# Performance work log

Measured on AMD Instinct MI355X. Metric: run time of the kernel, lower is better.

## Reference

```python
import jax, jax.numpy as jnp
import numpy as np

EPS = 1e-8  # torch CosineSimilarity eps


def setup_inputs() -> dict:
    key = jax.random.key(0)
    ks = jax.random.split(key, 7)
    N, D, H = 8192, 3, 256
    return {
        "pattern1": jax.random.normal(ks[0], (D,), jnp.float32),
        "pattern2": jax.random.normal(ks[1], (D,), jnp.float32),
        "working_memory": jax.random.normal(ks[2], (N, D), jnp.float32),
        "Wp": jax.random.normal(ks[3], (H, D), jnp.float32) * 0.1,
        "bp": jax.random.normal(ks[4], (H,), jnp.float32) * 0.1,
        "Wq": jax.random.normal(ks[5], (H, D), jnp.float32) * 0.1,
        "bq": jax.random.normal(ks[6], (H,), jnp.float32) * 0.1,
    }


def reference(pattern1, pattern2, working_memory, Wp, bp, Wq, bq):
    # Embed patterns and all propositions (torch Linear: x @ W.T + b)
    p1 = pattern1 @ Wp.T + bp                       # (H,)
    p2 = pattern2 @ Wp.T + bp                       # (H,)
    props = working_memory @ Wq.T + bq              # (N, H)
    prop_norm = jnp.linalg.norm(props, axis=-1)     # (N,)

    def match(pemb):
        # sigmoid(cosine_sim(pemb, props))  -> (N,)
        num = props @ pemb
        den = jnp.maximum(prop_norm * jnp.linalg.norm(pemb), EPS)
        return jax.nn.sigmoid(num / den)

    m1 = match(p1)                                  # (N,)
    m2 = match(p2)                                  # (N,)

    # Entity-link: cosine sim of scalar wm[i,2] with wm[j,0]
    obj = working_memory[:, 2]                      # (N,)
    subj = working_memory[:, 0]                     # (N,)
    num = obj[:, None] * subj[None, :]              # (N, N)
    den = jnp.maximum(jnp.abs(obj)[:, None] * jnp.abs(subj)[None, :], EPS)
    link = jax.nn.sigmoid(num / den)                # (N, N)

    out = m1[:, None] * m2[None, :] * link          # (N, N)
    N = out.shape[0]
    # zero the diagonal (i != j in the original loop)
    return out * (1.0 - jnp.eye(N, dtype=out.dtype))
```

## Files before the change

kernel.cpp:

```cpp
#include <hip/hip_runtime.h>
#include <math.h>

#define EPS 1e-8f
constexpr int N = 8192;
constexpr int ROWS_PER_BLOCK = 8;
constexpr int COLS_PER_BLOCK = 1024;
constexpr float LPOS = 0.7310585786300049f;
constexpr float LNEG = 0.2689414213699951f;

__global__ __launch_bounds__(256) void match_kernel(
    const float* __restrict__ pat1, const float* __restrict__ pat2,
    const float* __restrict__ Wp, const float* __restrict__ bp,
    const float* __restrict__ wm, const float* __restrict__ Wq,
    const float* __restrict__ bq,
    float4* __restrict__ rowpack, float* __restrict__ m2,
    float* __restrict__ subj) {
  const int row = (blockIdx.x * blockDim.x + threadIdx.x) >> 6;
  const int lane = threadIdx.x & 63;
  const float a0 = pat1[0], a1 = pat1[1], a2 = pat1[2];
  const float b0 = pat2[0], b1 = pat2[1], b2 = pat2[2];
  const float x0 = wm[row * 3 + 0];
  const float x1 = wm[row * 3 + 1];
  const float x2 = wm[row * 3 + 2];
  float s0 = 0.f, s1 = 0.f, s2 = 0.f, n1 = 0.f, n2 = 0.f;
#pragma unroll
  for (int k = 0; k < 4; ++k) {
    const int h = lane + k * 64;
    const float wp0 = Wp[h * 3 + 0], wp1 = Wp[h * 3 + 1], wp2 = Wp[h * 3 + 2];
    const float bph = bp[h];
    const float v1 = fmaf(wp0, a0, fmaf(wp1, a1, fmaf(wp2, a2, bph)));
    const float v2 = fmaf(wp0, b0, fmaf(wp1, b1, fmaf(wp2, b2, bph)));
    const float v  = fmaf(Wq[h * 3 + 0], x0,
                     fmaf(Wq[h * 3 + 1], x1,
                     fmaf(Wq[h * 3 + 2], x2, bq[h])));
    s0 = fmaf(v, v, s0);
    s1 = fmaf(v, v1, s1);
    s2 = fmaf(v, v2, s2);
    n1 = fmaf(v1, v1, n1);
    n2 = fmaf(v2, v2, n2);
  }
#pragma unroll
  for (int off = 32; off > 0; off >>= 1) {
    s0 += __shfl_xor(s0, off, 64);
    s1 += __shfl_xor(s1, off, 64);
    s2 += __shfl_xor(s2, off, 64);
    n1 += __shfl_xor(n1, off, 64);
    n2 += __shfl_xor(n2, off, 64);
  }
  if (lane == 0) {
    const float pn = sqrtf(s0);
    const float d1 = fmaxf(pn * sqrtf(n1), EPS);
    const float d2 = fmaxf(pn * sqrtf(n2), EPS);
    const float mm1 = 1.f / (1.f + __expf(-(s1 / d1)));
    const float mm2 = 1.f / (1.f + __expf(-(s2 / d2)));
    m2[row]   = mm2;
    subj[row] = x0;
    float4 rp;
    rp.x = mm1;
    rp.y = x2;
    rp.z = EPS / fabsf(x2);
    rp.w = 0.f;
    rowpack[row] = rp;
  }
}

__device__ __forceinline__ float exact_elem(float a, float oi, float m2c,
                                            float sjc) {
  const float t = oi * sjc;
  const float z = t / fmaxf(fabsf(t), EPS);
  return a * m2c * (1.f / (1.f + __expf(-z)));
}

__global__ __launch_bounds__(256) void outer_kernel(
    const float4* __restrict__ rowpack, const float* __restrict__ m2,
    const float* __restrict__ subj, float* __restrict__ out) {
  const int jBase = blockIdx.x * COLS_PER_BLOCK + threadIdx.x * 4;
  const int iBase = blockIdx.y * ROWS_PER_BLOCK;
  const float4 m2v = *reinterpret_cast<const float4*>(m2 + jBase);
  const float4 sjv = *reinterpret_cast<const float4*>(subj + jBase);
  float4 qp, qm, asj;
  qp.x = m2v.x * (sjv.x > 0.f ? LPOS : LNEG);
  qp.y = m2v.y * (sjv.y > 0.f ? LPOS : LNEG);
  qp.z = m2v.z * (sjv.z > 0.f ? LPOS : LNEG);
  qp.w = m2v.w * (sjv.w > 0.f ? LPOS : LNEG);
  qm.x = m2v.x * (sjv.x > 0.f ? LNEG : LPOS);
  qm.y = m2v.y * (sjv.y > 0.f ? LNEG : LPOS);
  qm.z = m2v.z * (sjv.z > 0.f ? LNEG : LPOS);
  qm.w = m2v.w * (sjv.w > 0.f ? LNEG : LPOS);
  asj.x = fabsf(sjv.x);
  asj.y = fabsf(sjv.y);
  asj.z = fabsf(sjv.z);
  asj.w = fabsf(sjv.w);
  const float minasj = fminf(fminf(asj.x, asj.y), fminf(asj.z, asj.w));
  const bool diagTile = (iBase >> 10) == (int)blockIdx.x;
#pragma unroll
  for (int r = 0; r < ROWS_PER_BLOCK; ++r) {
    const int i = iBase + r;
    const float4 rp = rowpack[i];
    const float a = rp.x, oi = rp.y, thr = rp.z;
    const bool neg = oi < 0.f;
    float4 o;
    o.x = a * (neg ? qm.x : qp.x);
    o.y = a * (neg ? qm.y : qp.y);
    o.z = a * (neg ? qm.z : qp.z);
    o.w = a * (neg ? qm.w : qp.w);
    if (__builtin_expect(__any(minasj < thr), 0)) {
      if (asj.x < thr) o.x = exact_elem(a, oi, m2v.x, sjv.x);
      if (asj.y < thr) o.y = exact_elem(a, oi, m2v.y, sjv.y);
      if (asj.z < thr) o.z = exact_elem(a, oi, m2v.z, sjv.z);
      if (asj.w < thr) o.w = exact_elem(a, oi, m2v.w, sjv.w);
    }
    if (diagTile) {
      if (jBase + 0 == i) o.x = 0.f;
      if (jBase + 1 == i) o.y = 0.f;
      if (jBase + 2 == i) o.z = 0.f;
      if (jBase + 3 == i) o.w = 0.f;
    }
    *reinterpret_cast<float4*>(out + (size_t)i * N + jBase) = o;
  }
}

extern "C" void kernel_launch(void* const* d_in, const int* in_sizes, int n_in,
                              void* d_out, int out_size, void* d_ws,
                              size_t ws_size, hipStream_t stream) {
  const float* pat1 = (const float*)d_in[0];
  const float* pat2 = (const float*)d_in[1];
  const float* wm   = (const float*)d_in[2];
  const float* Wp   = (const float*)d_in[3];
  const float* bp   = (const float*)d_in[4];
  const float* Wq   = (const float*)d_in[5];
  const float* bq   = (const float*)d_in[6];
  float* out = (float*)d_out;

  float4* rowpack = (float4*)d_ws;
  float* m2   = (float*)(rowpack + N);
  float* subj = m2 + N;

  match_kernel<<<N / 4, 256, 0, stream>>>(pat1, pat2, Wp, bp, wm, Wq, bq,
                                          rowpack, m2, subj);
  dim3 grid(N / COLS_PER_BLOCK, N / ROWS_PER_BLOCK);
  outer_kernel<<<grid, 256, 0, stream>>>(rowpack, m2, subj, out);
}
```

Before: 50.22 us.

## Restructure outer kernel to one block per output row

The outer-product kernel now gives each block a whole output row, looping over 8 column chunks of 1024. Previously each block handled 8 rows by 1024 columns and reused column data held in registers. Now each block reads the row scalars once and reloads the column vectors (m2, subj) from cache in every chunk. This trades column-data reuse in registers for a simpler per-row schedule and contiguous row writes. Output is 256MB and store-bound either way.

```diff
diff --git a/kernel.cpp b/kernel.cpp
--- a/kernel.cpp
+++ b/kernel.cpp
@@ -3,8 +3,6 @@
 
 #define EPS 1e-8f
 constexpr int N = 8192;
-constexpr int ROWS_PER_BLOCK = 8;
-constexpr int COLS_PER_BLOCK = 1024;
 constexpr float LPOS = 0.7310585786300049f;
 constexpr float LNEG = 0.2689414213699951f;
 
@@ -74,49 +72,39 @@
 __global__ __launch_bounds__(256) void outer_kernel(
     const float4* __restrict__ rowpack, const float* __restrict__ m2,
     const float* __restrict__ subj, float* __restrict__ out) {
-  const int jBase = blockIdx.x * COLS_PER_BLOCK + threadIdx.x * 4;
-  const int iBase = blockIdx.y * ROWS_PER_BLOCK;
-  const float4 m2v = *reinterpret_cast<const float4*>(m2 + jBase);
-  const float4 sjv = *reinterpret_cast<const float4*>(subj + jBase);
-  float4 qp, qm, asj;
-  qp.x = m2v.x * (sjv.x > 0.f ? LPOS : LNEG);
-  qp.y = m2v.y * (sjv.y > 0.f ? LPOS : LNEG);
-  qp.z = m2v.z * (sjv.z > 0.f ? LPOS : LNEG);
-  qp.w = m2v.w * (sjv.w > 0.f ? LPOS : LNEG);
-  qm.x = m2v.x * (sjv.x > 0.f ? LNEG : LPOS);
-  qm.y = m2v.y * (sjv.y > 0.f ? LNEG : LPOS);
-  qm.z = m2v.z * (sjv.z > 0.f ? LNEG : LPOS);
-  qm.w = m2v.w * (sjv.w > 0.f ? LNEG : LPOS);
-  asj.x = fabsf(sjv.x);
-  asj.y = fabsf(sjv.y);
-  asj.z = fabsf(sjv.z);
-  asj.w = fabsf(sjv.w);
-  const float minasj = fminf(fminf(asj.x, asj.y), fminf(asj.z, asj.w));
-  const bool diagTile = (iBase >> 10) == (int)blockIdx.x;
+  const int i = blockIdx.x;
+  const float4 rp = rowpack[i];
+  const float a = rp.x, oi = rp.y, thr = rp.z;
+  const float aLP = a * LPOS;
+  const float aLN = a * LNEG;
+  const bool neg = oi < 0.f;
+  float* __restrict__ outrow = out + (size_t)i * N;
+  const int t4 = threadIdx.x * 4;
 #pragma unroll
-  for (int r = 0; r < ROWS_PER_BLOCK; ++r) {
-    const int i = iBase + r;
-    const float4 rp = rowpack[i];
-    const float a = rp.x, oi = rp.y, thr = rp.z;
-    const bool neg = oi < 0.f;
+  for (int c = 0; c < N / 1024; ++c) {
+    const int j = c * 1024 + t4;
+    const float4 m2v = *reinterpret_cast<const float4*>(m2 + j);
+    const float4 sjv = *reinterpret_cast<const float4*>(subj + j);
     float4 o;
-    o.x = a * (neg ? qm.x : qp.x);
-    o.y = a * (neg ? qm.y : qp.y);
-    o.z = a * (neg ? qm.z : qp.z);
-    o.w = a * (neg ? qm.w : qp.w);
-    if (__builtin_expect(__any(minasj < thr), 0)) {
-      if (asj.x < thr) o.x = exact_elem(a, oi, m2v.x, sjv.x);
-      if (asj.y < thr) o.y = exact_elem(a, oi, m2v.y, sjv.y);
-      if (asj.z < thr) o.z = exact_elem(a, oi, m2v.z, sjv.z);
-      if (asj.w < thr) o.w = exact_elem(a, oi, m2v.w, sjv.w);
+    o.x = m2v.x * (((sjv.x > 0.f) != neg) ? aLP : aLN);
+    o.y = m2v.y * (((sjv.y > 0.f) != neg) ? aLP : aLN);
+    o.z = m2v.z * (((sjv.z > 0.f) != neg) ? aLP : aLN);
+    o.w = m2v.w * (((sjv.w > 0.f) != neg) ? aLP : aLN);
+    const float mn = fminf(fminf(fabsf(sjv.x), fabsf(sjv.y)),
+                           fminf(fabsf(sjv.z), fabsf(sjv.w)));
+    if (__builtin_expect(__any(mn < thr), 0)) {
+      if (fabsf(sjv.x) < thr) o.x = exact_elem(a, oi, m2v.x, sjv.x);
+      if (fabsf(sjv.y) < thr) o.y = exact_elem(a, oi, m2v.y, sjv.y);
+      if (fabsf(sjv.z) < thr) o.z = exact_elem(a, oi, m2v.z, sjv.z);
+      if (fabsf(sjv.w) < thr) o.w = exact_elem(a, oi, m2v.w, sjv.w);
     }
-    if (diagTile) {
-      if (jBase + 0 == i) o.x = 0.f;
-      if (jBase + 1 == i) o.y = 0.f;
-      if (jBase + 2 == i) o.z = 0.f;
-      if (jBase + 3 == i) o.w = 0.f;
+    if (__builtin_expect((unsigned)(i - j) < 4u, 0)) {
+      if (j + 0 == i) o.x = 0.f;
+      if (j + 1 == i) o.y = 0.f;
+      if (j + 2 == i) o.z = 0.f;
+      if (j + 3 == i) o.w = 0.f;
     }
-    *reinterpret_cast<float4*>(out + (size_t)i * N + jBase) = o;
+    *reinterpret_cast<float4*>(outrow + j) = o;
   }
 }
 
@@ -138,6 +126,5 @@
 
   match_kernel<<<N / 4, 256, 0, stream>>>(pat1, pat2, Wp, bp, wm, Wq, bq,
                                           rowpack, m2, subj);
-  dim3 grid(N / COLS_PER_BLOCK, N / ROWS_PER_BLOCK);
-  outer_kernel<<<grid, 256, 0, stream>>>(rowpack, m2, subj, out);
+  outer_kernel<<<N, 256, 0, stream>>>(rowpack, m2, subj, out);
 }
```

Result: no change. 51.10 us (+1.8%).

## Fuse match and outer kernels into one cooperative persistent kernel with grid sync

Applied to the files above, without the earlier changes.

Merges the match and outer-product kernels into a single cooperative launch of 1024 persistent blocks. Each block first computes row embeddings and match scores, then a grid-wide sync runs before it loops over output tiles in a grid-stride pattern. This removes the second kernel launch and the inter-kernel gap. In exchange it adds a grid barrier, the overhead of a cooperative launch, and less parallelism in the match phase, since each block now handles 8 rows.

```diff
diff --git a/kernel.cpp b/kernel.cpp
--- a/kernel.cpp
+++ b/kernel.cpp
@@ -1,68 +1,19 @@
 #include <hip/hip_runtime.h>
+#include <hip/hip_cooperative_groups.h>
 #include <math.h>
+
+namespace cg = cooperative_groups;
 
 #define EPS 1e-8f
 constexpr int N = 8192;
-constexpr int ROWS_PER_BLOCK = 8;
-constexpr int COLS_PER_BLOCK = 1024;
+constexpr int NBLOCKS = 1024;
+constexpr int ROWS_PER_TILE = 8;
+constexpr int COLS_PER_TILE = 1024;
+constexpr int NSTRIPES = N / COLS_PER_TILE;
+constexpr int NTILES = (N / ROWS_PER_TILE) * NSTRIPES;
+constexpr int TILES_PER_BLOCK = NTILES / NBLOCKS;
 constexpr float LPOS = 0.7310585786300049f;
 constexpr float LNEG = 0.2689414213699951f;
-
-__global__ __launch_bounds__(256) void match_kernel(
-    const float* __restrict__ pat1, const float* __restrict__ pat2,
-    const float* __restrict__ Wp, const float* __restrict__ bp,
-    const float* __restrict__ wm, const float* __restrict__ Wq,
-    const float* __restrict__ bq,
-    float4* __restrict__ rowpack, float* __restrict__ m2,
-    float* __restrict__ subj) {
-  const int row = (blockIdx.x * blockDim.x + threadIdx.x) >> 6;
-  const int lane = threadIdx.x & 63;
-  const float a0 = pat1[0], a1 = pat1[1], a2 = pat1[2];
-  const float b0 = pat2[0], b1 = pat2[1], b2 = pat2[2];
-  const float x0 = wm[row * 3 + 0];
-  const float x1 = wm[row * 3 + 1];
-  const float x2 = wm[row * 3 + 2];
-  float s0 = 0.f, s1 = 0.f, s2 = 0.f, n1 = 0.f, n2 = 0.f;
-#pragma unroll
-  for (int k = 0; k < 4; ++k) {
-    const int h = lane + k * 64;
-    const float wp0 = Wp[h * 3 + 0], wp1 = Wp[h * 3 + 1], wp2 = Wp[h * 3 + 2];
-    const float bph = bp[h];
-    const float v1 = fmaf(wp0, a0, fmaf(wp1, a1, fmaf(wp2, a2, bph)));
-    const float v2 = fmaf(wp0, b0, fmaf(wp1, b1, fmaf(wp2, b2, bph)));
-    const float v  = fmaf(Wq[h * 3 + 0], x0,
-                     fmaf(Wq[h * 3 + 1], x1,
-                     fmaf(Wq[h * 3 + 2], x2, bq[h])));
-    s0 = fmaf(v, v, s0);
-    s1 = fmaf(v, v1, s1);
-    s2 = fmaf(v, v2, s2);
-    n1 = fmaf(v1, v1, n1);
-    n2 = fmaf(v2, v2, n2);
-  }
-#pragma unroll
-  for (int off = 32; off > 0; off >>= 1) {
-    s0 += __shfl_xor(s0, off, 64);
-    s1 += __shfl_xor(s1, off, 64);
-    s2 += __shfl_xor(s2, off, 64);
-    n1 += __shfl_xor(n1, off, 64);
-    n2 += __shfl_xor(n2, off, 64);
-  }
-  if (lane == 0) {
-    const float pn = sqrtf(s0);
-    const float d1 = fmaxf(pn * sqrtf(n1), EPS);
-    const float d2 = fmaxf(pn * sqrtf(n2), EPS);
-    const float mm1 = 1.f / (1.f + __expf(-(s1 / d1)));
-    const float mm2 = 1.f / (1.f + __expf(-(s2 / d2)));
-    m2[row]   = mm2;
-    subj[row] = x0;
-    float4 rp;
-    rp.x = mm1;
-    rp.y = x2;
-    rp.z = EPS / fabsf(x2);
-    rp.w = 0.f;
-    rowpack[row] = rp;
-  }
-}
 
 __device__ __forceinline__ float exact_elem(float a, float oi, float m2c,
                                             float sjc) {
@@ -71,52 +22,121 @@
   return a * m2c * (1.f / (1.f + __expf(-z)));
 }
 
-__global__ __launch_bounds__(256) void outer_kernel(
-    const float4* __restrict__ rowpack, const float* __restrict__ m2,
-    const float* __restrict__ subj, float* __restrict__ out) {
-  const int jBase = blockIdx.x * COLS_PER_BLOCK + threadIdx.x * 4;
-  const int iBase = blockIdx.y * ROWS_PER_BLOCK;
-  const float4 m2v = *reinterpret_cast<const float4*>(m2 + jBase);
-  const float4 sjv = *reinterpret_cast<const float4*>(subj + jBase);
-  float4 qp, qm, asj;
-  qp.x = m2v.x * (sjv.x > 0.f ? LPOS : LNEG);
-  qp.y = m2v.y * (sjv.y > 0.f ? LPOS : LNEG);
-  qp.z = m2v.z * (sjv.z > 0.f ? LPOS : LNEG);
-  qp.w = m2v.w * (sjv.w > 0.f ? LPOS : LNEG);
-  qm.x = m2v.x * (sjv.x > 0.f ? LNEG : LPOS);
-  qm.y = m2v.y * (sjv.y > 0.f ? LNEG : LPOS);
-  qm.z = m2v.z * (sjv.z > 0.f ? LNEG : LPOS);
-  qm.w = m2v.w * (sjv.w > 0.f ? LNEG : LPOS);
-  asj.x = fabsf(sjv.x);
-  asj.y = fabsf(sjv.y);
-  asj.z = fabsf(sjv.z);
-  asj.w = fabsf(sjv.w);
-  const float minasj = fminf(fminf(asj.x, asj.y), fminf(asj.z, asj.w));
-  const bool diagTile = (iBase >> 10) == (int)blockIdx.x;
+__global__ __launch_bounds__(256, 4) void fused_kernel(
+    const float* __restrict__ pat1, const float* __restrict__ pat2,
+    const float* __restrict__ Wp, const float* __restrict__ bp,
+    const float* __restrict__ wm, const float* __restrict__ Wq,
+    const float* __restrict__ bq,
+    float4* __restrict__ rowpack, float* __restrict__ m2arr,
+    float* __restrict__ subjarr, float* __restrict__ out) {
+  const int wid = threadIdx.x >> 6;
+  const int lane = threadIdx.x & 63;
+
+  {
+    const float a0 = pat1[0], a1 = pat1[1], a2 = pat1[2];
+    const float b0 = pat2[0], b1 = pat2[1], b2 = pat2[2];
 #pragma unroll
-  for (int r = 0; r < ROWS_PER_BLOCK; ++r) {
-    const int i = iBase + r;
-    const float4 rp = rowpack[i];
-    const float a = rp.x, oi = rp.y, thr = rp.z;
-    const bool neg = oi < 0.f;
-    float4 o;
-    o.x = a * (neg ? qm.x : qp.x);
-    o.y = a * (neg ? qm.y : qp.y);
-    o.z = a * (neg ? qm.z : qp.z);
-    o.w = a * (neg ? qm.w : qp.w);
-    if (__builtin_expect(__any(minasj < thr), 0)) {
-      if (asj.x < thr) o.x = exact_elem(a, oi, m2v.x, sjv.x);
-      if (asj.y < thr) o.y = exact_elem(a, oi, m2v.y, sjv.y);
-      if (asj.z < thr) o.z = exact_elem(a, oi, m2v.z, sjv.z);
-      if (asj.w < thr) o.w = exact_elem(a, oi, m2v.w, sjv.w);
+    for (int rr = 0; rr < 2; ++rr) {
+      const int row = blockIdx.x * 8 + rr * 4 + wid;
+      const float x0 = wm[row * 3 + 0];
+      const float x1 = wm[row * 3 + 1];
+      const float x2 = wm[row * 3 + 2];
+      float s0 = 0.f, s1 = 0.f, s2 = 0.f, n1 = 0.f, n2 = 0.f;
+#pragma unroll
+      for (int k = 0; k < 4; ++k) {
+        const int h = lane + k * 64;
+        const float wp0 = Wp[h * 3 + 0], wp1 = Wp[h * 3 + 1],
+                    wp2 = Wp[h * 3 + 2];
+        const float bph = bp[h];
+        const float v1 = fmaf(wp0, a0, fmaf(wp1, a1, fmaf(wp2, a2, bph)));
+        const float v2 = fmaf(wp0, b0, fmaf(wp1, b1, fmaf(wp2, b2, bph)));
+        const float v  = fmaf(Wq[h * 3 + 0], x0,
+                         fmaf(Wq[h * 3 + 1], x1,
+                         fmaf(Wq[h * 3 + 2], x2, bq[h])));
+        s0 = fmaf(v, v, s0);
+        s1 = fmaf(v, v1, s1);
+        s2 = fmaf(v, v2, s2);
+        n1 = fmaf(v1, v1, n1);
+        n2 = fmaf(v2, v2, n2);
+      }
+#pragma unroll
+      for (int off = 32; off > 0; off >>= 1) {
+        s0 += __shfl_xor(s0, off, 64);
+        s1 += __shfl_xor(s1, off, 64);
+        s2 += __shfl_xor(s2, off, 64);
+        n1 += __shfl_xor(n1, off, 64);
+        n2 += __shfl_xor(n2, off, 64);
+      }
+      if (lane == 0) {
+        const float pn = sqrtf(s0);
+        const float d1 = fmaxf(pn * sqrtf(n1), EPS);
+        const float d2 = fmaxf(pn * sqrtf(n2), EPS);
+        const float mm1 = 1.f / (1.f + __expf(-(s1 / d1)));
+        const float mm2 = 1.f / (1.f + __expf(-(s2 / d2)));
+        m2arr[row]   = mm2;
+        subjarr[row] = x0;
+        float4 rp;
+        rp.x = mm1;
+        rp.y = x2;
+        rp.z = EPS / fabsf(x2);
+        rp.w = 0.f;
+        rowpack[row] = rp;
+      }
     }
-    if (diagTile) {
-      if (jBase + 0 == i) o.x = 0.f;
-      if (jBase + 1 == i) o.y = 0.f;
-      if (jBase + 2 == i) o.z = 0.f;
-      if (jBase + 3 == i) o.w = 0.f;
+  }
+
+  __threadfence();
+  cg::this_grid().sync();
+
+#pragma unroll 1
+  for (int k = 0; k < TILES_PER_BLOCK; ++k) {
+    const int t = blockIdx.x + k * NBLOCKS;
+    const int bx = t & (NSTRIPES - 1);
+    const int by = t >> 3;
+    const int jBase = bx * COLS_PER_TILE + (int)threadIdx.x * 4;
+    const int iBase = by * ROWS_PER_TILE;
+    const float4 m2v = *reinterpret_cast<const float4*>(m2arr + jBase);
+    const float4 sjv = *reinterpret_cast<const float4*>(subjarr + jBase);
+    float4 qp, qm, asj;
+    qp.x = m2v.x * (sjv.x > 0.f ? LPOS : LNEG);
+    qp.y = m2v.y * (sjv.y > 0.f ? LPOS : LNEG);
+    qp.z = m2v.z * (sjv.z > 0.f ? LPOS : LNEG);
+    qp.w = m2v.w * (sjv.w > 0.f ? LPOS : LNEG);
+    qm.x = m2v.x * (sjv.x > 0.f ? LNEG : LPOS);
+    qm.y = m2v.y * (sjv.y > 0.f ? LNEG : LPOS);
+    qm.z = m2v.z * (sjv.z > 0.f ? LNEG : LPOS);
+    qm.w = m2v.w * (sjv.w > 0.f ? LNEG : LPOS);
+    asj.x = fabsf(sjv.x);
+    asj.y = fabsf(sjv.y);
+    asj.z = fabsf(sjv.z);
+    asj.w = fabsf(sjv.w);
+    const float minasj = fminf(fminf(asj.x, asj.y), fminf(asj.z, asj.w));
+    const bool diagTile = (iBase >> 10) == bx;
+#pragma unroll
+    for (int r = 0; r < ROWS_PER_TILE; ++r) {
+      const int i = iBase + r;
+      const float4 rp = rowpack[i];
+      const float a = rp.x, oi = rp.y, thr = rp.z;
+      const bool neg = oi < 0.f;
+      float4 o;
+      o.x = a * (neg ? qm.x : qp.x);
+      o.y = a * (neg ? qm.y : qp.y);
+      o.z = a * (neg ? qm.z : qp.z);
+      o.w = a * (neg ? qm.w : qp.w);
+      if (__builtin_expect(__any(minasj < thr), 0)) {
+        if (asj.x < thr) o.x = exact_elem(a, oi, m2v.x, sjv.x);
+        if (asj.y < thr) o.y = exact_elem(a, oi, m2v.y, sjv.y);
+        if (asj.z < thr) o.z = exact_elem(a, oi, m2v.z, sjv.z);
+        if (asj.w < thr) o.w = exact_elem(a, oi, m2v.w, sjv.w);
+      }
+      if (diagTile) {
+        if (jBase + 0 == i) o.x = 0.f;
+        if (jBase + 1 == i) o.y = 0.f;
+        if (jBase + 2 == i) o.z = 0.f;
+        if (jBase + 3 == i) o.w = 0.f;
+      }
+      *reinterpret_cast<float4*>(out + (size_t)i * N + jBase) = o;
     }
-    *reinterpret_cast<float4*>(out + (size_t)i * N + jBase) = o;
   }
 }
 
@@ -136,8 +156,8 @@
   float* m2   = (float*)(rowpack + N);
   float* subj = m2 + N;
 
-  match_kernel<<<N / 4, 256, 0, stream>>>(pat1, pat2, Wp, bp, wm, Wq, bq,
-                                          rowpack, m2, subj);
-  dim3 grid(N / COLS_PER_BLOCK, N / ROWS_PER_BLOCK);
-  outer_kernel<<<grid, 256, 0, stream>>>(rowpack, m2, subj, out);
+  void* args[] = {&pat1, &pat2, &Wp, &bp, &wm, &Wq, &bq,
+                  &rowpack, &m2, &subj, &out};
+  hipLaunchCooperativeKernel(reinterpret_cast<const void*>(&fused_kernel),
+                             dim3(NBLOCKS), dim3(256), args, 0, stream);
 }
```

Result: slower. 181.3 us (+261.0%).
